# Kernel tuning notes

Measured on AMD Instinct MI355X. Metric: run time of the kernel, lower is better.

The kernel has to match this reference:

```python
import jax, jax.numpy as jnp
import numpy as np

B, N = 128, 1024


def setup_inputs() -> dict:
    key = jax.random.key(0)
    k1, k2 = jax.random.split(key)
    vector = jax.random.uniform(k1, (B, N), dtype=jnp.float32)
    interactions = jax.random.normal(k2, (N, N), dtype=jnp.float32)
    return {"vector": vector, "interactions": interactions}


def reference(vector, interactions):
    # x: [B,1,N], y: [B,N,1] -> broadcast dirac delta [B,N,N]
    x = vector[:, None, :]
    y = vector[:, :, None]
    dd = (1.0 - x) * (1.0 - y) + x * y  # [B,N,N]
    dd = jnp.triu(dd)                   # keep upper triangle incl. diagonal
    energy = dd * interactions          # [B,N,N] * [N,N] broadcast
    return energy.reshape(vector.shape[0], -1).sum(axis=1)  # [B]
```

## Files before the change

### kernel.cpp

```cpp
#include <hip/hip_runtime.h>
#include <math.h>

#define NDIM 1024
#define BDIM 128
#define TS 32
#define NT (NDIM / TS)
#define NTILES (NT * (NT + 1) / 2)
#define NHALF (NTILES * 2)
#define R1B 16
#define ROWS_PER_R1 (NHALF / R1B)

__global__ __launch_bounds__(128) void potts_main(
    const float* __restrict__ V,
    const float* __restrict__ W,
    float* __restrict__ partial)
{
    const int t2 = blockIdx.x;
    const int t = t2 >> 1, half = t2 & 1;
    const int u = NTILES - 1 - t;
    int kk = (int)(0.5f * (sqrtf((float)(8 * u + 1)) - 1.0f));
    if (kk * (kk + 1) / 2 > u) --kk;
    if ((kk + 1) * (kk + 2) / 2 <= u) ++kk;
    const int ti = NT - 1 - kk;
    const int tj = NT - 1 - (u - kk * (kk + 1) / 2);
    const int rbase = 16 * half;
    const int I0h = ti * TS + rbase;
    const int J0 = tj * TS;
    const bool diag = (ti == tj);

    __shared__ float wt[16][36];
    __shared__ float rs[16];
    __shared__ float vjt[TS][130];
    __shared__ float vit[16][130];
    __shared__ float red[2][BDIM];

    const int tid = threadIdx.x;
    const int w = tid >> 6;
    const int l = tid & 63;

    {
        const int r = tid >> 3, c4 = (tid & 7) * 4;
        float4 w4 = *(const float4*)(W + (size_t)(I0h + r) * NDIM + (J0 + c4));
        if (diag) {
            const int lr = rbase + r;
            if (c4 + 0 < lr) w4.x = 0.0f;
            if (c4 + 1 < lr) w4.y = 0.0f;
            if (c4 + 2 < lr) w4.z = 0.0f;
            if (c4 + 3 < lr) w4.w = 0.0f;
        }
        *(float4*)(&wt[r][c4]) = w4;
        float rsum = (w4.x + w4.y) + (w4.z + w4.w);
        rsum += __shfl_xor(rsum, 1);
        rsum += __shfl_xor(rsum, 2);
        rsum += __shfl_xor(rsum, 4);
        if ((tid & 7) == 0) rs[r] = rsum;
    }

#pragma unroll
    for (int it = 0; it < 8; ++it) {
        const int fid = tid + 128 * it;
        const int b = fid >> 3, c4 = (fid & 7) * 4;
        const float4 a = *(const float4*)(V + (size_t)b * NDIM + (J0 + c4));
        vjt[c4 + 0][b] = a.x; vjt[c4 + 1][b] = a.y;
        vjt[c4 + 2][b] = a.z; vjt[c4 + 3][b] = a.w;
    }
#pragma unroll
    for (int it = 0; it < 4; ++it) {
        const int fid = tid + 128 * it;
        const int b = fid >> 2, c4 = (fid & 3) * 4;
        const float4 a = *(const float4*)(V + (size_t)b * NDIM + (I0h + c4));
        vit[c4 + 0][b] = a.x; vit[c4 + 1][b] = a.y;
        vit[c4 + 2][b] = a.z; vit[c4 + 3][b] = a.w;
    }
    __syncthreads();

    float vj0[TS], vj1[TS];
#pragma unroll
    for (int j = 0; j < TS; ++j) {
        vj0[j] = vjt[j][l];
        vj1[j] = vjt[j][l + 64];
    }

    float acc0 = 0.0f, acc1 = 0.0f;
#pragma unroll
    for (int k = 0; k < 8; ++k) {
        const int il = 8 * w + k;
        const float vi0 = vit[il][l], vi1 = vit[il][l + 64];
        const float* wrow = &wt[il][0];
        float za0 = 0.f, zb0 = 0.f, za1 = 0.f, zb1 = 0.f;
#pragma unroll
        for (int j4 = 0; j4 < 8; j4 += 2) {
            const float4 wa = *(const float4*)(wrow + 4 * j4);
            const float4 wb = *(const float4*)(wrow + 4 * j4 + 4);
            za0 = fmaf(wa.x, vj0[4 * j4 + 0], za0);
            za0 = fmaf(wa.y, vj0[4 * j4 + 1], za0);
            za0 = fmaf(wa.z, vj0[4 * j4 + 2], za0);
            za0 = fmaf(wa.w, vj0[4 * j4 + 3], za0);
            za1 = fmaf(wa.x, vj1[4 * j4 + 0], za1);
            za1 = fmaf(wa.y, vj1[4 * j4 + 1], za1);
            za1 = fmaf(wa.z, vj1[4 * j4 + 2], za1);
            za1 = fmaf(wa.w, vj1[4 * j4 + 3], za1);
            zb0 = fmaf(wb.x, vj0[4 * j4 + 4], zb0);
            zb0 = fmaf(wb.y, vj0[4 * j4 + 5], zb0);
            zb0 = fmaf(wb.z, vj0[4 * j4 + 6], zb0);
            zb0 = fmaf(wb.w, vj0[4 * j4 + 7], zb0);
            zb1 = fmaf(wb.x, vj1[4 * j4 + 4], zb1);
            zb1 = fmaf(wb.y, vj1[4 * j4 + 5], zb1);
            zb1 = fmaf(wb.z, vj1[4 * j4 + 6], zb1);
            zb1 = fmaf(wb.w, vj1[4 * j4 + 7], zb1);
        }
        const float rsk = rs[il];
        acc0 = fmaf(1.0f - vi0, rsk, acc0);
        acc0 = fmaf(2.0f * vi0 - 1.0f, za0 + zb0, acc0);
        acc1 = fmaf(1.0f - vi1, rsk, acc1);
        acc1 = fmaf(2.0f * vi1 - 1.0f, za1 + zb1, acc1);
    }

    red[w][l] = acc0;
    red[w][l + 64] = acc1;
    __syncthreads();
    if (tid < BDIM) {
        partial[(size_t)t2 * BDIM + tid] = red[0][tid] + red[1][tid];
    }
}

__global__ __launch_bounds__(256) void potts_red1(
    const float* __restrict__ partial, float* __restrict__ ws2)
{
    const int g = blockIdx.x;
    const int tid = threadIdx.x;
    const int b = tid & 127, h = tid >> 7;
    const float* __restrict__ base = partial + (size_t)g * ROWS_PER_R1 * BDIM;
    float a = 0.0f;
#pragma unroll
    for (int kx = 0; kx < ROWS_PER_R1 / 2; ++kx)
        a += base[(size_t)(2 * kx + h) * BDIM + b];
    __shared__ float s[256];
    s[tid] = a;
    __syncthreads();
    if (tid < BDIM) ws2[g * BDIM + tid] = s[tid] + s[tid + BDIM];
}

__global__ __launch_bounds__(256) void potts_red2(
    const float* __restrict__ ws2, float* __restrict__ out)
{
    const int tid = threadIdx.x;
    const int b = tid & 127, h = tid >> 7;
    float a = 0.0f;
#pragma unroll
    for (int g = 0; g < R1B / 2; ++g)
        a += ws2[(2 * g + h) * BDIM + b];
    __shared__ float s[256];
    s[tid] = a;
    __syncthreads();
    if (tid < BDIM) out[tid] = s[tid] + s[tid + BDIM];
}

extern "C" void kernel_launch(void* const* d_in, const int* in_sizes, int n_in,
                              void* d_out, int out_size, void* d_ws, size_t ws_size,
                              hipStream_t stream) {
    const float* V = (const float*)d_in[0];
    const float* W = (const float*)d_in[1];
    float* out = (float*)d_out;
    float* partial = (float*)d_ws;
    float* ws2 = partial + (size_t)NHALF * BDIM;

    potts_main<<<dim3(NHALF), dim3(128), 0, stream>>>(V, W, partial);
    potts_red1<<<dim3(R1B), dim3(256), 0, stream>>>(partial, ws2);
    potts_red2<<<dim3(1), dim3(256), 0, stream>>>(ws2, out);
}
```

Measured before the change: 64.85 us.

## Add prep kernel for transposed V and upper-triangular row sums

Adds a prep kernel that writes a transposed copy of V (N x B) to workspace and computes the upper-triangular row sums of W. The main kernel then drops its shared-memory staging and barriers, loading vj and vi straight from the transposed buffer with coalesced loads and reading W directly. The linear term is added once per row on diagonal tiles instead of once per tile. The cost is an extra kernel launch and a round trip through global memory, plus heavier register use per thread.

```diff
diff --git a/kernel.cpp b/kernel.cpp
--- a/kernel.cpp
+++ b/kernel.cpp
@@ -10,9 +10,70 @@
 #define R1B 16
 #define ROWS_PER_R1 (NHALF / R1B)
 
-__global__ __launch_bounds__(128) void potts_main(
+#define OFF_WS2 (NHALF * BDIM)
+#define OFF_VT  (OFF_WS2 + R1B * BDIM)
+#define OFF_R   (OFF_VT + NDIM * BDIM)
+
+
+__global__ __launch_bounds__(256) void potts_prep(
     const float* __restrict__ V,
     const float* __restrict__ W,
+    float* __restrict__ VT,
+    float* __restrict__ R)
+{
+    __shared__ float tr[TS][BDIM + 2];
+    const int bid = blockIdx.x;
+    const int tid = threadIdx.x;
+
+    if (bid < 256) {
+        const int wv = tid >> 6, l = tid & 63;
+        const int i = 4 * bid + wv;
+        const float* __restrict__ row = W + (size_t)i * NDIM;
+        float s = 0.0f;
+#pragma unroll
+        for (int it = 0; it < 4; ++it) {
+            const int c = 4 * l + 256 * it;
+            float4 a = *(const float4*)(row + c);
+            if (c + 0 < i) a.x = 0.0f;
+            if (c + 1 < i) a.y = 0.0f;
+            if (c + 2 < i) a.z = 0.0f;
+            if (c + 3 < i) a.w = 0.0f;
+            s += (a.x + a.y) + (a.z + a.w);
+        }
+        s += __shfl_xor(s, 1);
+        s += __shfl_xor(s, 2);
+        s += __shfl_xor(s, 4);
+        s += __shfl_xor(s, 8);
+        s += __shfl_xor(s, 16);
+        s += __shfl_xor(s, 32);
+        if (l == 0) R[i] = s;
+    } else {
+        const int J0 = 32 * (bid - 256);
+#pragma unroll
+        for (int it = 0; it < 4; ++it) {
+            const int fid = tid + 256 * it;
+            const int b = fid >> 3, c4 = (fid & 7) * 4;
+            const float4 a = *(const float4*)(V + (size_t)b * NDIM + J0 + c4);
+            tr[c4 + 0][b] = a.x; tr[c4 + 1][b] = a.y;
+            tr[c4 + 2][b] = a.z; tr[c4 + 3][b] = a.w;
+        }
+        __syncthreads();
+#pragma unroll
+        for (int it = 0; it < 4; ++it) {
+            const int fid = tid + 256 * it;
+            const int j = fid >> 5, b4 = (fid & 31) * 4;
+            float4 o;
+            o.x = tr[j][b4 + 0]; o.y = tr[j][b4 + 1];
+            o.z = tr[j][b4 + 2]; o.w = tr[j][b4 + 3];
+            *(float4*)(VT + (size_t)(J0 + j) * BDIM + b4) = o;
+        }
+    }
+}
+
+__global__ __launch_bounds__(128) void potts_main(
+    const float* __restrict__ W,
+    const float* __restrict__ VT,
+    const float* __restrict__ R,
     float* __restrict__ partial)
 {
     const int t2 = blockIdx.x;
@@ -28,100 +89,56 @@
     const int J0 = tj * TS;
     const bool diag = (ti == tj);
 
-    __shared__ float wt[16][36];
-    __shared__ float rs[16];
-    __shared__ float vjt[TS][130];
-    __shared__ float vit[16][130];
-    __shared__ float red[2][BDIM];
+    const int tid = threadIdx.x;
 
-    const int tid = threadIdx.x;
-    const int w = tid >> 6;
-    const int l = tid & 63;
+    float vj[TS];
+#pragma unroll
+    for (int j = 0; j < TS; ++j)
+        vj[j] = VT[(size_t)(J0 + j) * BDIM + tid];
+    float vi[16];
+#pragma unroll
+    for (int il = 0; il < 16; ++il)
+        vi[il] = VT[(size_t)(I0h + il) * BDIM + tid];
 
-    {
-        const int r = tid >> 3, c4 = (tid & 7) * 4;
-        float4 w4 = *(const float4*)(W + (size_t)(I0h + r) * NDIM + (J0 + c4));
-        if (diag) {
-            const int lr = rbase + r;
-            if (c4 + 0 < lr) w4.x = 0.0f;
-            if (c4 + 1 < lr) w4.y = 0.0f;
-            if (c4 + 2 < lr) w4.z = 0.0f;
-            if (c4 + 3 < lr) w4.w = 0.0f;
-        }
-        *(float4*)(&wt[r][c4]) = w4;
-        float rsum = (w4.x + w4.y) + (w4.z + w4.w);
-        rsum += __shfl_xor(rsum, 1);
-        rsum += __shfl_xor(rsum, 2);
-        rsum += __shfl_xor(rsum, 4);
-        if ((tid & 7) == 0) rs[r] = rsum;
+    float acc = 0.0f;
+    if (diag) {
+#pragma unroll
+        for (int il = 0; il < 16; ++il)
+            acc = fmaf(1.0f - vi[il], R[I0h + il], acc);
     }
 
 #pragma unroll
-    for (int it = 0; it < 8; ++it) {
-        const int fid = tid + 128 * it;
-        const int b = fid >> 3, c4 = (fid & 7) * 4;
-        const float4 a = *(const float4*)(V + (size_t)b * NDIM + (J0 + c4));
-        vjt[c4 + 0][b] = a.x; vjt[c4 + 1][b] = a.y;
-        vjt[c4 + 2][b] = a.z; vjt[c4 + 3][b] = a.w;
-    }
+    for (int il = 0; il < 16; ++il) {
+        const float* __restrict__ wr = W + (size_t)(I0h + il) * NDIM + J0;
+        float za = 0.f, zb = 0.f;
 #pragma unroll
-    for (int it = 0; it < 4; ++it) {
-        const int fid = tid + 128 * it;
-        const int b = fid >> 2, c4 = (fid & 3) * 4;
-        const float4 a = *(const float4*)(V + (size_t)b * NDIM + (I0h + c4));
-        vit[c4 + 0][b] = a.x; vit[c4 + 1][b] = a.y;
-        vit[c4 + 2][b] = a.z; vit[c4 + 3][b] = a.w;
-    }
-    __syncthreads();
-
-    float vj0[TS], vj1[TS];
-#pragma unroll
-    for (int j = 0; j < TS; ++j) {
-        vj0[j] = vjt[j][l];
-        vj1[j] = vjt[j][l + 64];
+        for (int j4 = 0; j4 < 8; j4 += 2) {
+            float4 wa = *(const float4*)(wr + 4 * j4);
+            float4 wb = *(const float4*)(wr + 4 * j4 + 4);
+            if (diag) {
+                const int lr = rbase + il;
+                if (4 * j4 + 0 < lr) wa.x = 0.0f;
+                if (4 * j4 + 1 < lr) wa.y = 0.0f;
+                if (4 * j4 + 2 < lr) wa.z = 0.0f;
+                if (4 * j4 + 3 < lr) wa.w = 0.0f;
+                if (4 * j4 + 4 < lr) wb.x = 0.0f;
+                if (4 * j4 + 5 < lr) wb.y = 0.0f;
+                if (4 * j4 + 6 < lr) wb.z = 0.0f;
+                if (4 * j4 + 7 < lr) wb.w = 0.0f;
+            }
+            za = fmaf(wa.x, vj[4 * j4 + 0], za);
+            za = fmaf(wa.y, vj[4 * j4 + 1], za);
+            za = fmaf(wa.z, vj[4 * j4 + 2], za);
+            za = fmaf(wa.w, vj[4 * j4 + 3], za);
+            zb = fmaf(wb.x, vj[4 * j4 + 4], zb);
+            zb = fmaf(wb.y, vj[4 * j4 + 5], zb);
+            zb = fmaf(wb.z, vj[4 * j4 + 6], zb);
+            zb = fmaf(wb.w, vj[4 * j4 + 7], zb);
+        }
+        acc = fmaf(2.0f * vi[il] - 1.0f, za + zb, acc);
     }
 
-    float acc0 = 0.0f, acc1 = 0.0f;
-#pragma unroll
-    for (int k = 0; k < 8; ++k) {
-        const int il = 8 * w + k;
-        const float vi0 = vit[il][l], vi1 = vit[il][l + 64];
-        const float* wrow = &wt[il][0];
-        float za0 = 0.f, zb0 = 0.f, za1 = 0.f, zb1 = 0.f;
-#pragma unroll
-        for (int j4 = 0; j4 < 8; j4 += 2) {
-            const float4 wa = *(const float4*)(wrow + 4 * j4);
-            const float4 wb = *(const float4*)(wrow + 4 * j4 + 4);
-            za0 = fmaf(wa.x, vj0[4 * j4 + 0], za0);
-            za0 = fmaf(wa.y, vj0[4 * j4 + 1], za0);
-            za0 = fmaf(wa.z, vj0[4 * j4 + 2], za0);
-            za0 = fmaf(wa.w, vj0[4 * j4 + 3], za0);
-            za1 = fmaf(wa.x, vj1[4 * j4 + 0], za1);
-            za1 = fmaf(wa.y, vj1[4 * j4 + 1], za1);
-            za1 = fmaf(wa.z, vj1[4 * j4 + 2], za1);
-            za1 = fmaf(wa.w, vj1[4 * j4 + 3], za1);
-            zb0 = fmaf(wb.x, vj0[4 * j4 + 4], zb0);
-            zb0 = fmaf(wb.y, vj0[4 * j4 + 5], zb0);
-            zb0 = fmaf(wb.z, vj0[4 * j4 + 6], zb0);
-            zb0 = fmaf(wb.w, vj0[4 * j4 + 7], zb0);
-            zb1 = fmaf(wb.x, vj1[4 * j4 + 4], zb1);
-            zb1 = fmaf(wb.y, vj1[4 * j4 + 5], zb1);
-            zb1 = fmaf(wb.z, vj1[4 * j4 + 6], zb1);
-            zb1 = fmaf(wb.w, vj1[4 * j4 + 7], zb1);
-        }
-        const float rsk = rs[il];
-        acc0 = fmaf(1.0f - vi0, rsk, acc0);
-        acc0 = fmaf(2.0f * vi0 - 1.0f, za0 + zb0, acc0);
-        acc1 = fmaf(1.0f - vi1, rsk, acc1);
-        acc1 = fmaf(2.0f * vi1 - 1.0f, za1 + zb1, acc1);
-    }
-
-    red[w][l] = acc0;
-    red[w][l + 64] = acc1;
-    __syncthreads();
-    if (tid < BDIM) {
-        partial[(size_t)t2 * BDIM + tid] = red[0][tid] + red[1][tid];
-    }
+    partial[(size_t)t2 * BDIM + tid] = acc;
 }
 
 __global__ __launch_bounds__(256) void potts_red1(
@@ -162,10 +179,14 @@
     const float* V = (const float*)d_in[0];
     const float* W = (const float*)d_in[1];
     float* out = (float*)d_out;
-    float* partial = (float*)d_ws;
-    float* ws2 = partial + (size_t)NHALF * BDIM;
+    float* ws = (float*)d_ws;
+    float* partial = ws;
+    float* ws2 = ws + OFF_WS2;
+    float* VT = ws + OFF_VT;
+    float* R  = ws + OFF_R;
 
-    potts_main<<<dim3(NHALF), dim3(128), 0, stream>>>(V, W, partial);
+    potts_prep<<<dim3(288), dim3(256), 0, stream>>>(V, W, VT, R);
+    potts_main<<<dim3(NHALF), dim3(128), 0, stream>>>(W, VT, R, partial);
     potts_red1<<<dim3(R1B), dim3(256), 0, stream>>>(partial, ws2);
     potts_red2<<<dim3(1), dim3(256), 0, stream>>>(ws2, out);
 }
```

New measurement: 101.6 us. +56.7%, slower.
